# Kernel tuning notes

Measured on AMD Instinct MI355X. Metric: run time of the kernel, lower is better.

## Reference

```python
import jax, jax.numpy as jnp
import numpy as np

N_NODES = 20000
N_EDGES = 640000
D_NODE = 128
D_EDGE = 64
D_OUT = 128


def setup_inputs() -> dict:
    key = jax.random.key(0)
    ks = jax.random.split(key, 7)
    feats_node = jax.random.normal(ks[0], (N_NODES, D_NODE), dtype=jnp.float32)
    feats_edge = jax.random.normal(ks[1], (N_EDGES, D_EDGE), dtype=jnp.float32)
    # nn.init.normal_(std=0.5) on all three linear weights
    Wn = 0.5 * jax.random.normal(ks[2], (D_OUT, D_NODE), dtype=jnp.float32)
    We = 0.5 * jax.random.normal(ks[3], (D_OUT, D_EDGE), dtype=jnp.float32)
    Wa = 0.5 * jax.random.normal(ks[4], (1, 3 * D_OUT), dtype=jnp.float32)
    src = jax.random.randint(ks[5], (N_EDGES,), 0, N_NODES, dtype=jnp.int32)
    dst = jax.random.randint(ks[6], (N_EDGES,), 0, N_NODES, dtype=jnp.int32)
    return {"feats_node": feats_node, "feats_edge": feats_edge,
            "Wn": Wn, "We": We, "Wa": Wa, "src": src, "dst": dst}


def reference(feats_node, feats_edge, Wn, We, Wa, src, dst):
    n_nodes = feats_node.shape[0]
    d = Wn.shape[0]
    # dense projections: z_node [N, d], z_edge [E, d]
    z_node = feats_node @ Wn.T
    z_edge = feats_edge @ We.T
    # split attn weight so we never materialize the [E, 3d] concat
    a_src, a_dst, a_e = Wa[0, :d], Wa[0, d:2 * d], Wa[0, 2 * d:]
    z_src = z_node[src]                       # [E, d] gather
    z_dst = z_node[dst]                       # [E, d] gather
    logits = z_src @ a_src + z_dst @ a_dst + z_edge @ a_e   # [E]
    e = jax.nn.leaky_relu(logits, negative_slope=0.2)
    # segment softmax over incoming edges of each dst node
    m = jax.ops.segment_max(e, dst, num_segments=n_nodes)   # [N]
    ex = jnp.exp(e - m[dst])                                 # [E]
    s = jax.ops.segment_sum(ex, dst, num_segments=n_nodes)  # [N]
    alpha = ex / jnp.where(s[dst] == 0, 1.0, s[dst])         # [E]
    # weighted scatter-sum of src features into dst nodes
    h = jax.ops.segment_sum(alpha[:, None] * z_src, dst, num_segments=n_nodes)
    return h
```

## Files before the change

kernel.cpp:

```cpp
#include <hip/hip_runtime.h>
#include <hip/hip_bf16.h>

#define N_NODES 20000
#define N_EDGES 640000
#define D_NODE  128
#define D_EDGE  64
#define D_OUT   128

__device__ __forceinline__ unsigned short f2bf(float x) {
    unsigned u = __float_as_uint(x);
    unsigned r = ((u >> 16) & 1u) + 0x7FFFu;
    return (unsigned short)((u + r) >> 16);
}
__device__ __forceinline__ float bf2f(unsigned short b) {
    return __uint_as_float((unsigned)b << 16);
}

__global__ __launch_bounds__(256) void k_init_prep(const float* __restrict__ Wn,
                                                   const float* __restrict__ We,
                                                   const float* __restrict__ Wa,
                                                   int* __restrict__ deg,
                                                   float* __restrict__ WnT,
                                                   float* __restrict__ ce) {
    int t = threadIdx.x, b = blockIdx.x;
    int gid = b * 256 + t;
    if (gid < N_NODES) deg[gid] = 0;
    if (gid < D_OUT * D_NODE) {
        int o = gid >> 7, k = gid & 127;
        WnT[k * D_OUT + o] = Wn[gid];
    }
    if (b == 79) {
        __shared__ float tmp[256];
        int e = t & 63, p = t >> 6;
        float a = 0.f;
#pragma unroll
        for (int oo = 0; oo < 32; ++oo) {
            int o = p * 32 + oo;
            a += Wa[2 * D_OUT + o] * We[o * D_EDGE + e];
        }
        tmp[t] = a;
        __syncthreads();
        if (t < 64) ce[t] = tmp[t] + tmp[t + 64] + tmp[t + 128] + tmp[t + 192];
    }
}

__global__ __launch_bounds__(256) void k_fused(const float* __restrict__ feats,
                                               const float* __restrict__ wT,
                                               const float* __restrict__ Wa,
                                               const float* __restrict__ fe,
                                               const float* __restrict__ ce,
                                               const int* __restrict__ dst,
                                               unsigned short* __restrict__ zb,
                                               float* __restrict__ ssrc,
                                               float* __restrict__ sdst,
                                               int* __restrict__ deg,
                                               int* __restrict__ rank,
                                               float* __restrict__ ge) {
    __shared__ float sW[32 * 128];
    __shared__ float sF[32 * 128];
    int t = threadIdx.x;

    if (blockIdx.x >= 625) {
        int b = blockIdx.x - 625;
        int part = t & 3;
        const float4* c4 = (const float4*)(ce + part * 16);
        float4 c0 = c4[0], c1 = c4[1], c2 = c4[2], c3 = c4[3];
#pragma unroll
        for (int chunk = 0; chunk < 4; ++chunk) {
            int j = b * 256 + chunk * 64 + (t >> 2);
            const float4* row = (const float4*)(fe + (size_t)j * D_EDGE + part * 16);
            float4 f0 = row[0], f1 = row[1], f2 = row[2], f3 = row[3];
            float acc = f0.x * c0.x + f0.y * c0.y + f0.z * c0.z + f0.w * c0.w
                      + f1.x * c1.x + f1.y * c1.y + f1.z * c1.z + f1.w * c1.w
                      + f2.x * c2.x + f2.y * c2.y + f2.z * c2.z + f2.w * c2.w
                      + f3.x * c3.x + f3.y * c3.y + f3.z * c3.z + f3.w * c3.w;
            acc += __shfl_xor(acc, 1, 64);
            acc += __shfl_xor(acc, 2, 64);
            if (part == 0) {
                ge[j] = acc;
                rank[j] = atomicAdd(&deg[dst[j]], 1);
            }
        }
        return;
    }

    int nb = blockIdx.x * 32;
    const float4* fsrc = (const float4*)(feats + (size_t)nb * D_NODE);
    float4* fdst = (float4*)sF;
    for (int i = t; i < 32 * 32; i += 256) fdst[i] = fsrc[i];

    float acc[4][4] = {{0.f}};
    int o0 = (t & 31) * 4;
    int n0 = (t >> 5) * 4;

    for (int p = 0; p < 4; ++p) {
        __syncthreads();
        const float4* wsrc = (const float4*)(wT + p * 32 * 128);
        float4* wdst = (float4*)sW;
        for (int i = t; i < 32 * 32; i += 256) wdst[i] = wsrc[i];
        __syncthreads();
        for (int kk = 0; kk < 32; kk += 4) {
            float4 w0 = *(const float4*)(sW + (kk + 0) * 128 + o0);
            float4 w1 = *(const float4*)(sW + (kk + 1) * 128 + o0);
            float4 w2 = *(const float4*)(sW + (kk + 2) * 128 + o0);
            float4 w3 = *(const float4*)(sW + (kk + 3) * 128 + o0);
#pragma unroll
            for (int j = 0; j < 4; ++j) {
                float4 f = *(const float4*)(sF + (n0 + j) * 128 + p * 32 + kk);
                acc[j][0] += f.x * w0.x + f.y * w1.x + f.z * w2.x + f.w * w3.x;
                acc[j][1] += f.x * w0.y + f.y * w1.y + f.z * w2.y + f.w * w3.y;
                acc[j][2] += f.x * w0.z + f.y * w1.z + f.z * w2.z + f.w * w3.z;
                acc[j][3] += f.x * w0.w + f.y * w1.w + f.z * w2.w + f.w * w3.w;
            }
        }
    }

    float as0 = Wa[o0 + 0], as1 = Wa[o0 + 1], as2 = Wa[o0 + 2], as3 = Wa[o0 + 3];
    float ad0 = Wa[128 + o0 + 0], ad1 = Wa[128 + o0 + 1],
          ad2 = Wa[128 + o0 + 2], ad3 = Wa[128 + o0 + 3];
#pragma unroll
    for (int j = 0; j < 4; ++j) {
        int n = nb + n0 + j;
        ushort4 zo;
        zo.x = f2bf(acc[j][0]); zo.y = f2bf(acc[j][1]);
        zo.z = f2bf(acc[j][2]); zo.w = f2bf(acc[j][3]);
        *(ushort4*)(zb + (size_t)n * D_OUT + o0) = zo;
        float ps = acc[j][0] * as0 + acc[j][1] * as1 + acc[j][2] * as2 + acc[j][3] * as3;
        float pd = acc[j][0] * ad0 + acc[j][1] * ad1 + acc[j][2] * ad2 + acc[j][3] * ad3;
#pragma unroll
        for (int off = 16; off; off >>= 1) {
            ps += __shfl_xor(ps, off, 32);
            pd += __shfl_xor(pd, off, 32);
        }
        if ((t & 31) == 0) { ssrc[n] = ps; sdst[n] = pd; }
    }
}

__global__ __launch_bounds__(1024) void k_scan(const int* __restrict__ deg,
                                               int* __restrict__ offsets) {
    __shared__ int wsum[16];
    __shared__ int woff[16];
    const int PER = 20;
    int t = threadIdx.x, lane = t & 63, wv = t >> 6;
    int base = t * PER;
    int v[PER];
    int tsum = 0;
#pragma unroll
    for (int i = 0; i < PER; ++i) {
        int idx = base + i;
        v[i] = (idx < N_NODES) ? deg[idx] : 0;
        tsum += v[i];
    }
    int x = tsum;
#pragma unroll
    for (int d = 1; d < 64; d <<= 1) {
        int y = __shfl_up(x, d, 64);
        if (lane >= d) x += y;
    }
    if (lane == 63) wsum[wv] = x;
    __syncthreads();
    if (t == 0) {
        int a = 0;
        for (int i = 0; i < 16; ++i) { int tmp = wsum[i]; woff[i] = a; a += tmp; }
        offsets[N_NODES] = a;
    }
    __syncthreads();
    int run = (x - tsum) + woff[wv];
#pragma unroll
    for (int i = 0; i < PER; ++i) {
        int idx = base + i;
        if (idx < N_NODES) offsets[idx] = run;
        run += v[i];
    }
}

__global__ __launch_bounds__(256) void k_place(const float* __restrict__ ge,
                                               const float* __restrict__ ssrc,
                                               const float* __restrict__ sdst,
                                               const int* __restrict__ src,
                                               const int* __restrict__ dst,
                                               const int* __restrict__ rank,
                                               const int* __restrict__ offsets,
                                               float2* __restrict__ es) {
    int j = blockIdx.x * 256 + threadIdx.x;
    int sj = src[j], dj = dst[j];
    float x = ge[j] + ssrc[sj] + sdst[dj];
    float ev = x > 0.f ? x : 0.2f * x;
    int pos = offsets[dj] + rank[j];
    es[pos] = make_float2(ev, __int_as_float(sj));
}

__global__ __launch_bounds__(256) void k_gather(const int* __restrict__ offsets,
                                                const float2* __restrict__ es,
                                                const unsigned short* __restrict__ zb,
                                                float* __restrict__ h) {
    int lane = threadIdx.x & 63;
    int n = blockIdx.x * 4 + (threadIdx.x >> 6);
    int beg = offsets[n], end = offsets[n + 1];

    float2 v0 = make_float2(-3.4e38f, 0.f);
    int i0 = beg + lane;
    if (i0 < end) v0 = es[i0];
    float lmax = v0.x;
    for (int base = beg + 64; base < end; base += 64) {
        int i = base + lane;
        lmax = fmaxf(lmax, (i < end) ? es[i].x : -3.4e38f);
    }
#pragma unroll
    for (int off = 32; off; off >>= 1) lmax = fmaxf(lmax, __shfl_xor(lmax, off, 64));
    float m = lmax;

    float w0 = (i0 < end) ? __expf(v0.x - m) : 0.f;
    float lsum = w0;
    for (int base = beg + 64; base < end; base += 64) {
        int i = base + lane;
        lsum += (i < end) ? __expf(es[i].x - m) : 0.f;
    }
#pragma unroll
    for (int off = 32; off; off >>= 1) lsum += __shfl_xor(lsum, off, 64);
    float inv = (lsum > 0.f) ? 1.f / lsum : 0.f;

    float accx = 0.f, accy = 0.f;
    {
        int cnt = min(64, end - beg);
        float wl = w0 * inv;
        int sl = __float_as_int(v0.y);
        int r = 0;
        for (; r + 4 <= cnt; r += 4) {
            float wr0 = __shfl(wl, r + 0, 64); int sr0 = __shfl(sl, r + 0, 64);
            float wr1 = __shfl(wl, r + 1, 64); int sr1 = __shfl(sl, r + 1, 64);
            float wr2 = __shfl(wl, r + 2, 64); int sr2 = __shfl(sl, r + 2, 64);
            float wr3 = __shfl(wl, r + 3, 64); int sr3 = __shfl(sl, r + 3, 64);
            ushort2 z0 = *(const ushort2*)(zb + (size_t)sr0 * D_OUT + lane * 2);
            ushort2 z1 = *(const ushort2*)(zb + (size_t)sr1 * D_OUT + lane * 2);
            ushort2 z2 = *(const ushort2*)(zb + (size_t)sr2 * D_OUT + lane * 2);
            ushort2 z3 = *(const ushort2*)(zb + (size_t)sr3 * D_OUT + lane * 2);
            accx += wr0 * bf2f(z0.x) + wr1 * bf2f(z1.x) + wr2 * bf2f(z2.x) + wr3 * bf2f(z3.x);
            accy += wr0 * bf2f(z0.y) + wr1 * bf2f(z1.y) + wr2 * bf2f(z2.y) + wr3 * bf2f(z3.y);
        }
        for (; r < cnt; ++r) {
            float wr = __shfl(wl, r, 64); int sr = __shfl(sl, r, 64);
            ushort2 zv = *(const ushort2*)(zb + (size_t)sr * D_OUT + lane * 2);
            accx += wr * bf2f(zv.x); accy += wr * bf2f(zv.y);
        }
    }
    for (int base = beg + 64; base < end; base += 64) {
        int i = base + lane;
        float2 v = (i < end) ? es[i] : make_float2(0.f, 0.f);
        float wl = (i < end) ? __expf(v.x - m) * inv : 0.f;
        int sl = __float_as_int(v.y);
        int cnt = min(64, end - base);
        int r = 0;
        for (; r + 4 <= cnt; r += 4) {
            float wr0 = __shfl(wl, r + 0, 64); int sr0 = __shfl(sl, r + 0, 64);
            float wr1 = __shfl(wl, r + 1, 64); int sr1 = __shfl(sl, r + 1, 64);
            float wr2 = __shfl(wl, r + 2, 64); int sr2 = __shfl(sl, r + 2, 64);
            float wr3 = __shfl(wl, r + 3, 64); int sr3 = __shfl(sl, r + 3, 64);
            ushort2 z0 = *(const ushort2*)(zb + (size_t)sr0 * D_OUT + lane * 2);
            ushort2 z1 = *(const ushort2*)(zb + (size_t)sr1 * D_OUT + lane * 2);
            ushort2 z2 = *(const ushort2*)(zb + (size_t)sr2 * D_OUT + lane * 2);
            ushort2 z3 = *(const ushort2*)(zb + (size_t)sr3 * D_OUT + lane * 2);
            accx += wr0 * bf2f(z0.x) + wr1 * bf2f(z1.x) + wr2 * bf2f(z2.x) + wr3 * bf2f(z3.x);
            accy += wr0 * bf2f(z0.y) + wr1 * bf2f(z1.y) + wr2 * bf2f(z2.y) + wr3 * bf2f(z3.y);
        }
        for (; r < cnt; ++r) {
            float wr = __shfl(wl, r, 64); int sr = __shfl(sl, r, 64);
            ushort2 zv = *(const ushort2*)(zb + (size_t)sr * D_OUT + lane * 2);
            accx += wr * bf2f(zv.x); accy += wr * bf2f(zv.y);
        }
    }
    *(float2*)(h + (size_t)n * D_OUT + lane * 2) = make_float2(accx, accy);
}

extern "C" void kernel_launch(void* const* d_in, const int* in_sizes, int n_in,
                              void* d_out, int out_size, void* d_ws, size_t ws_size,
                              hipStream_t stream) {
    const float* feats_node = (const float*)d_in[0];
    const float* feats_edge = (const float*)d_in[1];
    const float* Wn = (const float*)d_in[2];
    const float* We = (const float*)d_in[3];
    const float* Wa = (const float*)d_in[4];
    const int* src = (const int*)d_in[5];
    const int* dst = (const int*)d_in[6];
    float* h = (float*)d_out;

    float* WnT  = (float*)d_ws;
    float* ce   = WnT + 16384;
    float* ssrc = ce + 64;
    float* sdst = ssrc + N_NODES;
    float2* es  = (float2*)(sdst + N_NODES);
    unsigned short* zb = (unsigned short*)(es + N_EDGES);
    int* deg     = (int*)(zb + (size_t)N_NODES * D_OUT);
    int* offsets = deg + N_NODES;
    int* rank    = offsets + N_NODES + 1;
    float* ge    = (float*)(rank + N_EDGES);

    k_init_prep<<<80, 256, 0, stream>>>(Wn, We, Wa, deg, WnT, ce);
    k_fused<<<3125, 256, 0, stream>>>(feats_node, WnT, Wa, feats_edge, ce,
                                      dst, zb, ssrc, sdst, deg, rank, ge);
    k_scan<<<1, 1024, 0, stream>>>(deg, offsets);
    k_place<<<N_EDGES / 256, 256, 0, stream>>>(ge, ssrc, sdst, src, dst, rank, offsets, es);
    k_gather<<<N_NODES / 4, 256, 0, stream>>>(offsets, es, zb, h);
}
```

Baseline: 312.9 us.

## Gather four edges per wave with 16-byte row loads and fuse sum into gather

The gather kernel now splits each 64-lane wave into four 16-lane groups, each loading a full 256-byte bf16 source row with uint4 loads, so four edges are processed per iteration. Partial accumulators are combined with cross-group shuffles at the end. The softmax denominator is accumulated in the same pass as the weighted sum, and normalisation is applied once at the end, removing one pass over the edge list. The cost is eight accumulators per lane, extra shuffles, and masked tail iterations.

```diff
diff --git a/kernel.cpp b/kernel.cpp
--- a/kernel.cpp
+++ b/kernel.cpp
@@ -198,11 +198,8 @@
     int n = blockIdx.x * 4 + (threadIdx.x >> 6);
     int beg = offsets[n], end = offsets[n + 1];
 
-    float2 v0 = make_float2(-3.4e38f, 0.f);
-    int i0 = beg + lane;
-    if (i0 < end) v0 = es[i0];
-    float lmax = v0.x;
-    for (int base = beg + 64; base < end; base += 64) {
+    float lmax = -3.4e38f;
+    for (int base = beg; base < end; base += 64) {
         int i = base + lane;
         lmax = fmaxf(lmax, (i < end) ? es[i].x : -3.4e38f);
     }
@@ -210,66 +207,47 @@
     for (int off = 32; off; off >>= 1) lmax = fmaxf(lmax, __shfl_xor(lmax, off, 64));
     float m = lmax;
 
-    float w0 = (i0 < end) ? __expf(v0.x - m) : 0.f;
-    float lsum = w0;
-    for (int base = beg + 64; base < end; base += 64) {
+    float lsum = 0.f;
+    float acc[8] = {0.f, 0.f, 0.f, 0.f, 0.f, 0.f, 0.f, 0.f};
+    int g = lane >> 4;
+    int c = (lane & 15) * 8;
+    for (int base = beg; base < end; base += 64) {
         int i = base + lane;
-        lsum += (i < end) ? __expf(es[i].x - m) : 0.f;
+        float2 v = (i < end) ? es[i] : make_float2(0.f, 0.f);
+        float wl = (i < end) ? __expf(v.x - m) : 0.f;
+        lsum += wl;
+        int sl = __float_as_int(v.y);
+        int cnt = min(64, end - base);
+        for (int r = 0; r < cnt; r += 4) {
+            int rr = r + g;
+            float wr = __shfl(wl, rr, 64);
+            if (rr >= cnt) wr = 0.f;
+            int sr = __shfl(sl, rr, 64);
+            uint4 z = *(const uint4*)(zb + (size_t)sr * D_OUT + c);
+            acc[0] += wr * __uint_as_float(z.x << 16);
+            acc[1] += wr * __uint_as_float(z.x & 0xFFFF0000u);
+            acc[2] += wr * __uint_as_float(z.y << 16);
+            acc[3] += wr * __uint_as_float(z.y & 0xFFFF0000u);
+            acc[4] += wr * __uint_as_float(z.z << 16);
+            acc[5] += wr * __uint_as_float(z.z & 0xFFFF0000u);
+            acc[6] += wr * __uint_as_float(z.w << 16);
+            acc[7] += wr * __uint_as_float(z.w & 0xFFFF0000u);
+        }
     }
 #pragma unroll
     for (int off = 32; off; off >>= 1) lsum += __shfl_xor(lsum, off, 64);
     float inv = (lsum > 0.f) ? 1.f / lsum : 0.f;
 
-    float accx = 0.f, accy = 0.f;
-    {
-        int cnt = min(64, end - beg);
-        float wl = w0 * inv;
-        int sl = __float_as_int(v0.y);
-        int r = 0;
-        for (; r + 4 <= cnt; r += 4) {
-            float wr0 = __shfl(wl, r + 0, 64); int sr0 = __shfl(sl, r + 0, 64);
-            float wr1 = __shfl(wl, r + 1, 64); int sr1 = __shfl(sl, r + 1, 64);
-            float wr2 = __shfl(wl, r + 2, 64); int sr2 = __shfl(sl, r + 2, 64);
-            float wr3 = __shfl(wl, r + 3, 64); int sr3 = __shfl(sl, r + 3, 64);
-            ushort2 z0 = *(const ushort2*)(zb + (size_t)sr0 * D_OUT + lane * 2);
-            ushort2 z1 = *(const ushort2*)(zb + (size_t)sr1 * D_OUT + lane * 2);
-            ushort2 z2 = *(const ushort2*)(zb + (size_t)sr2 * D_OUT + lane * 2);
-            ushort2 z3 = *(const ushort2*)(zb + (size_t)sr3 * D_OUT + lane * 2);
-            accx += wr0 * bf2f(z0.x) + wr1 * bf2f(z1.x) + wr2 * bf2f(z2.x) + wr3 * bf2f(z3.x);
-            accy += wr0 * bf2f(z0.y) + wr1 * bf2f(z1.y) + wr2 * bf2f(z2.y) + wr3 * bf2f(z3.y);
-        }
-        for (; r < cnt; ++r) {
-            float wr = __shfl(wl, r, 64); int sr = __shfl(sl, r, 64);
-            ushort2 zv = *(const ushort2*)(zb + (size_t)sr * D_OUT + lane * 2);
-            accx += wr * bf2f(zv.x); accy += wr * bf2f(zv.y);
-        }
-    }
-    for (int base = beg + 64; base < end; base += 64) {
-        int i = base + lane;
-        float2 v = (i < end) ? es[i] : make_float2(0.f, 0.f);
-        float wl = (i < end) ? __expf(v.x - m) * inv : 0.f;
-        int sl = __float_as_int(v.y);
-        int cnt = min(64, end - base);
-        int r = 0;
-        for (; r + 4 <= cnt; r += 4) {
-            float wr0 = __shfl(wl, r + 0, 64); int sr0 = __shfl(sl, r + 0, 64);
-            float wr1 = __shfl(wl, r + 1, 64); int sr1 = __shfl(sl, r + 1, 64);
-            float wr2 = __shfl(wl, r + 2, 64); int sr2 = __shfl(sl, r + 2, 64);
-            float wr3 = __shfl(wl, r + 3, 64); int sr3 = __shfl(sl, r + 3, 64);
-            ushort2 z0 = *(const ushort2*)(zb + (size_t)sr0 * D_OUT + lane * 2);
-            ushort2 z1 = *(const ushort2*)(zb + (size_t)sr1 * D_OUT + lane * 2);
-            ushort2 z2 = *(const ushort2*)(zb + (size_t)sr2 * D_OUT + lane * 2);
-            ushort2 z3 = *(const ushort2*)(zb + (size_t)sr3 * D_OUT + lane * 2);
-            accx += wr0 * bf2f(z0.x) + wr1 * bf2f(z1.x) + wr2 * bf2f(z2.x) + wr3 * bf2f(z3.x);
-            accy += wr0 * bf2f(z0.y) + wr1 * bf2f(z1.y) + wr2 * bf2f(z2.y) + wr3 * bf2f(z3.y);
-        }
-        for (; r < cnt; ++r) {
-            float wr = __shfl(wl, r, 64); int sr = __shfl(sl, r, 64);
-            ushort2 zv = *(const ushort2*)(zb + (size_t)sr * D_OUT + lane * 2);
-            accx += wr * bf2f(zv.x); accy += wr * bf2f(zv.y);
-        }
-    }
-    *(float2*)(h + (size_t)n * D_OUT + lane * 2) = make_float2(accx, accy);
+#pragma unroll
+    for (int k = 0; k < 8; ++k) {
+        acc[k] += __shfl_xor(acc[k], 16, 64);
+        acc[k] += __shfl_xor(acc[k], 32, 64);
+        acc[k] *= inv;
+    }
+    if (lane < 16) {
+        *(float4*)(h + (size_t)n * D_OUT + c)     = make_float4(acc[0], acc[1], acc[2], acc[3]);
+        *(float4*)(h + (size_t)n * D_OUT + c + 4) = make_float4(acc[4], acc[5], acc[6], acc[7]);
+    }
 }
 
 extern "C" void kernel_launch(void* const* d_in, const int* in_sizes, int n_in,
```

Result: no change. 311.2 us (-0.5%).
